# Performance work log

Hardware: AMD Instinct MI355X
Metric: run time of the kernel (lower is better)

## Reference

```python
import jax, jax.numpy as jnp
import numpy as np

B, S, D, O, H, E, K = 4, 1024, 1024, 1024, 2048, 8, 2
EPS = 1e-5

def _layernorm(x, g, b):
    m = jnp.mean(x, axis=-1, keepdims=True)
    v = jnp.mean(jnp.square(x - m), axis=-1, keepdims=True)
    return (x - m) * jax.lax.rsqrt(v + EPS) * g + b

def setup_inputs() -> dict:
    key = jax.random.key(0)
    ks = jax.random.split(key, 8)
    def xavier(k, shape):
        fan_out, fan_in = shape[-2], shape[-1]
        bound = float(np.sqrt(6.0 / (fan_in + fan_out)))
        return jax.random.uniform(k, shape, jnp.float32, -bound, bound)
    return {
        "x": jax.random.normal(ks[0], (B, S, D), jnp.float32),
        "ln1_g": jnp.ones((D,), jnp.float32), "ln1_b": jnp.zeros((D,), jnp.float32),
        "router_w": xavier(ks[1], (E, D)), "router_b": jnp.zeros((E,), jnp.float32),
        "sh_w1": xavier(ks[2], (H, D)), "sh_b1": jnp.zeros((H,), jnp.float32),
        "sh_w2": xavier(ks[3], (O, H)), "sh_b2": jnp.zeros((O,), jnp.float32),
        "e_w1": xavier(ks[4], (E, H, D)), "e_b1": jnp.zeros((E, H), jnp.float32),
        "e_w2": xavier(ks[5], (E, O, H)), "e_b2": jnp.zeros((E, O), jnp.float32),
        "ln2_g": jnp.ones((O,), jnp.float32), "ln2_b": jnp.zeros((O,), jnp.float32),
    }

def reference(x, ln1_g, ln1_b, router_w, router_b, sh_w1, sh_b1, sh_w2, sh_b2,
              e_w1, e_b1, e_w2, e_b2, ln2_g, ln2_b):
    # eval mode: no router noise, no aux loss
    x_norm = _layernorm(x, ln1_g, ln1_b)               # [B,S,D]
    xf = x_norm.reshape(-1, D)                          # [T,D]
    logits = xf @ router_w.T + router_b                 # [T,E]
    probs = jax.nn.softmax(logits, axis=-1)
    tk_w, tk_i = jax.lax.top_k(probs, K)                # [T,K]
    tk_w = tk_w / jnp.sum(tk_w, axis=-1, keepdims=True)
    # shared expert (exact GELU, as torch nn.GELU default)
    shared = jax.nn.gelu(xf @ sh_w1.T + sh_b1, approximate=False) @ sh_w2.T + sh_b2  # [T,O]
    # all experts densely, combined sparsely by top-k weights
    hid = jax.nn.gelu(jnp.einsum('td,ehd->teh', xf, e_w1) + e_b1, approximate=False)  # [T,E,H]
    eout = jnp.einsum('teh,eoh->teo', hid, e_w2) + e_b2                                # [T,E,O]
    comb_w = jnp.sum(jax.nn.one_hot(tk_i, E, dtype=xf.dtype) * tk_w[..., None], axis=1)  # [T,E]
    out = shared * (1.0 / (E + 1)) + jnp.einsum('te,teo->to', comb_w, eout)           # [T,O]
    out = _layernorm(out.reshape(B, S, O), ln2_g, ln2_b)
    return out
```

## Files before the change

kernel.cpp:

```cpp
#include <hip/hip_runtime.h>
#include <math.h>
#include <stdint.h>

typedef unsigned short u16;
typedef unsigned int u32;

typedef __attribute__((ext_vector_type(8))) short bf16x8;
typedef __attribute__((ext_vector_type(4))) float f32x4;

#define ASYNC_COPY16(g, l)                                                         \
  __builtin_amdgcn_global_load_lds((__attribute__((address_space(1))) const void*)(g), \
                                   (__attribute__((address_space(3))) void*)(l), 16, 0, 0)

__device__ __forceinline__ float bf2f(u16 u) {
  union { u32 i; float f; } v; v.i = ((u32)u) << 16; return v.f;
}
__device__ __forceinline__ u16 f2bf(float f) {
  union { float f; u32 i; } v; v.f = f;
  u32 r = v.i + 0x7fffu + ((v.i >> 16) & 1u);
  return (u16)(r >> 16);
}

__global__ __launch_bounds__(256) void cvt_all_k(
    const float* __restrict__ s0, const float* __restrict__ s1,
    const float* __restrict__ s2, const float* __restrict__ s3,
    u16* __restrict__ dst)
{
  const int64_t i0 = (int64_t)blockIdx.x * 2048 + (int64_t)threadIdx.x * 8;
  const float* src; int64_t rel;
  if (i0 < 2097152)       { src = s0; rel = i0; }
  else if (i0 < 4194304)  { src = s1; rel = i0 - 2097152; }
  else if (i0 < 20971520) { src = s2; rel = i0 - 4194304; }
  else                    { src = s3; rel = i0 - 20971520; }
  const float4 a = *(const float4*)(src + rel);
  const float4 b = *(const float4*)(src + rel + 4);
  union { u16 h[8]; uint4 v; } o;
  o.h[0] = f2bf(a.x); o.h[1] = f2bf(a.y); o.h[2] = f2bf(a.z); o.h[3] = f2bf(a.w);
  o.h[4] = f2bf(b.x); o.h[5] = f2bf(b.y); o.h[6] = f2bf(b.z); o.h[7] = f2bf(b.w);
  *(uint4*)(dst + i0) = o.v;
}

__global__ __launch_bounds__(256) void ln_router_k(
    const float* __restrict__ x, const float* __restrict__ g, const float* __restrict__ b,
    const float* __restrict__ rw, const float* __restrict__ rb,
    u16* __restrict__ xn, int* __restrict__ tk_idx, float* __restrict__ tk_w)
{
  const int t = blockIdx.x, tid = threadIdx.x;
  __shared__ float xs[1024];
  __shared__ float red[8];
  __shared__ float logits[8];
  const int wave = tid >> 6, lane = tid & 63;

  const float4 xv = *(const float4*)(x + (size_t)t * 1024 + 4 * tid);
  float v0 = xv.x, v1 = xv.y, v2 = xv.z, v3 = xv.w;
  float s = v0 + v1 + v2 + v3;
  float q = v0 * v0 + v1 * v1 + v2 * v2 + v3 * v3;
#pragma unroll
  for (int o = 32; o > 0; o >>= 1) { s += __shfl_down(s, o, 64); q += __shfl_down(q, o, 64); }
  if (lane == 0) { red[wave] = s; red[4 + wave] = q; }
  __syncthreads();
  if (tid == 0) {
    float S = red[0] + red[1] + red[2] + red[3];
    float Q = red[4] + red[5] + red[6] + red[7];
    float mean = S * (1.0f / 1024.0f);
    float var = Q * (1.0f / 1024.0f) - mean * mean;
    red[0] = mean; red[1] = rsqrtf(var + 1e-5f);
  }
  __syncthreads();
  const float mean = red[0], rstd = red[1];
  float vv[4] = {v0, v1, v2, v3};
  union { u16 h[4]; uint2 v; } pk;
#pragma unroll
  for (int j = 0; j < 4; ++j) {
    int d = 4 * tid + j;
    float y = (vv[j] - mean) * rstd * g[d] + b[d];
    xs[d] = y;
    pk.h[j] = f2bf(y);
  }
  *(uint2*)(xn + (size_t)t * 1024 + 4 * tid) = pk.v;
  __syncthreads();
#pragma unroll
  for (int pe = 0; pe < 2; ++pe) {
    int e = wave + 4 * pe;
    const float* wrow = rw + (size_t)e * 1024;
    float acc = 0.f;
#pragma unroll
    for (int j = 0; j < 16; ++j) {
      int d = lane + 64 * j;
      acc += xs[d] * wrow[d];
    }
#pragma unroll
    for (int o = 32; o > 0; o >>= 1) acc += __shfl_down(acc, o, 64);
    if (lane == 0) logits[e] = acc + rb[e];
  }
  __syncthreads();
  if (tid == 0) {
    int i0 = 0; float l0 = logits[0];
#pragma unroll
    for (int e = 1; e < 8; ++e) if (logits[e] > l0) { l0 = logits[e]; i0 = e; }
    int i1 = -1; float l1 = -3.4e38f;
#pragma unroll
    for (int e = 0; e < 8; ++e) { if (e == i0) continue; if (logits[e] > l1) { l1 = logits[e]; i1 = e; } }
    float w0 = 1.0f / (1.0f + expf(l1 - l0));
    float w1 = 1.0f - w0;
    tk_idx[2 * t] = i0; tk_idx[2 * t + 1] = i1;
    tk_w[2 * t] = w0; tk_w[2 * t + 1] = w1;
  }
}

__device__ __forceinline__ uint4 u4_add(uint4 a, uint4 b) {
  uint4 r; r.x = a.x + b.x; r.y = a.y + b.y; r.z = a.z + b.z; r.w = a.w + b.w; return r;
}
__device__ __forceinline__ uint4 u4_sub(uint4 a, uint4 b) {
  uint4 r; r.x = a.x - b.x; r.y = a.y - b.y; r.z = a.z - b.z; r.w = a.w - b.w; return r;
}

__global__ __launch_bounds__(256) void assign_k(
    const int* __restrict__ tk_idx, const float* __restrict__ tk_w,
    int* __restrict__ offs, int* __restrict__ slot_token,
    float* __restrict__ slot_w, int* __restrict__ slot_of)
{
  const int tid = threadIdx.x, lane = tid & 63, wave = tid >> 6;
  int eidx[32];
#pragma unroll
  for (int j = 0; j < 32; ++j) eidx[j] = tk_idx[tid * 32 + j];

  uint4 p = {0u, 0u, 0u, 0u};
#pragma unroll
  for (int j = 0; j < 32; ++j) {
    int e = eidx[j];
    unsigned inc = 1u << ((e & 1) * 16);
    int c = e >> 1;
    if (c == 0) p.x += inc; else if (c == 1) p.y += inc;
    else if (c == 2) p.z += inc; else p.w += inc;
  }
  const uint4 own = p;
#pragma unroll
  for (int o = 1; o < 64; o <<= 1) {
    uint4 t;
    t.x = (u32)__shfl_up((int)p.x, o, 64);
    t.y = (u32)__shfl_up((int)p.y, o, 64);
    t.z = (u32)__shfl_up((int)p.z, o, 64);
    t.w = (u32)__shfl_up((int)p.w, o, 64);
    if (lane >= o) p = u4_add(p, t);
  }
  __shared__ uint4 wtot[4];
  __shared__ int offs_s[9];
  if (lane == 63) wtot[wave] = p;
  __syncthreads();
  uint4 wbase = {0u, 0u, 0u, 0u};
  uint4 gtot = {0u, 0u, 0u, 0u};
#pragma unroll
  for (int w2 = 0; w2 < 4; ++w2) {
    uint4 t = wtot[w2];
    if (w2 < wave) wbase = u4_add(wbase, t);
    gtot = u4_add(gtot, t);
  }
  const uint4 excl = u4_sub(p, own);
  if (tid == 0) {
    int gtots[8] = { (int)(gtot.x & 0xffff), (int)(gtot.x >> 16),
                     (int)(gtot.y & 0xffff), (int)(gtot.y >> 16),
                     (int)(gtot.z & 0xffff), (int)(gtot.z >> 16),
                     (int)(gtot.w & 0xffff), (int)(gtot.w >> 16) };
    int a = 0;
#pragma unroll
    for (int e = 0; e < 8; ++e) { offs_s[e] = a; offs[e] = a; a += gtots[e]; }
    offs_s[8] = a; offs[8] = a;
  }
  __syncthreads();
  const uint4 pre = u4_add(wbase, excl);
  int base[8];
  base[0] = offs_s[0] + (int)(pre.x & 0xffff);
  base[1] = offs_s[1] + (int)(pre.x >> 16);
  base[2] = offs_s[2] + (int)(pre.y & 0xffff);
  base[3] = offs_s[3] + (int)(pre.y >> 16);
  base[4] = offs_s[4] + (int)(pre.z & 0xffff);
  base[5] = offs_s[5] + (int)(pre.z >> 16);
  base[6] = offs_s[6] + (int)(pre.w & 0xffff);
  base[7] = offs_s[7] + (int)(pre.w >> 16);
#pragma unroll
  for (int j = 0; j < 32; ++j) {
    int idx = tid * 32 + j;
    int e = eidx[j];
    int s = base[e]++;
    slot_token[s] = idx >> 1;
    slot_w[s] = tk_w[idx];
    slot_of[idx] = s;
  }
}

template <int N, int KD, int STAGE>
__global__ __launch_bounds__(256) void gemm_fused_k(
    const u16* __restrict__ Abase, const u16* __restrict__ Bsh,
    const u16* __restrict__ Bex, const float* __restrict__ bias_sh,
    const float* __restrict__ bias_ex,
    float* __restrict__ outF, u16* __restrict__ outH,
    const int* __restrict__ offs, const int* __restrict__ slot_token,
    const float* __restrict__ slot_w)
{
  const int tid = threadIdx.x;
  const int z = blockIdx.z;
  int off = 0, cnt = 4096, obase = 0;
  const u16* B = Bsh;
  const float* biasp = bias_sh;
  if (z > 0) {
    off = offs[z - 1]; cnt = offs[z] - off; obase = 4096 + off;
    B = Bex + (size_t)(z - 1) * N * KD;
    biasp = bias_ex + (size_t)(z - 1) * N;
  }
  const int m0 = blockIdx.y * 128;
  if (m0 >= cnt) return;
  const int n0 = blockIdx.x * 128;

  __shared__ u16 lA[128 * 32];
  __shared__ u16 lB[128 * 32];

  const int rS = tid >> 2;
  const int c8 = (tid & 3) * 8;

  int ra0 = m0 + rS;      if (ra0 > cnt - 1) ra0 = cnt - 1;
  int ra1 = m0 + rS + 64; if (ra1 > cnt - 1) ra1 = cnt - 1;
  size_t arow0, arow1;
  if (STAGE == 1) {
    if (z == 0) { arow0 = (size_t)ra0; arow1 = (size_t)ra1; }
    else        { arow0 = (size_t)slot_token[off + ra0]; arow1 = (size_t)slot_token[off + ra1]; }
  } else {
    if (z == 0) { arow0 = (size_t)ra0; arow1 = (size_t)ra1; }
    else        { arow0 = (size_t)(4096 + off + ra0); arow1 = (size_t)(4096 + off + ra1); }
  }
  const u16* gA0 = Abase + arow0 * KD + c8;
  const u16* gA1 = Abase + arow1 * KD + c8;
  const u16* gB0 = B + (size_t)(n0 + rS) * KD + c8;
  const u16* gB1 = B + (size_t)(n0 + rS + 64) * KD + c8;

  const int wave = tid >> 6, lane = tid & 63;
  u16* lA_w0 = lA + wave * 512;
  u16* lA_w1 = lA + 2048 + wave * 512;
  u16* lB_w0 = lB + wave * 512;
  u16* lB_w1 = lB + 2048 + wave * 512;

  const int wr = wave >> 1, wc = wave & 1;
  const int fr = lane & 15, fq = lane >> 4;
  const u16* rdA = lA + (wr * 64 + fr) * 32 + fq * 8;
  const u16* rdB = lB + (wc * 64 + fr) * 32 + fq * 8;

  f32x4 acc[4][4];
  const f32x4 zero = {0.f, 0.f, 0.f, 0.f};
#pragma unroll
  for (int i = 0; i < 4; ++i)
#pragma unroll
    for (int n = 0; n < 4; ++n) acc[i][n] = zero;

  const int NK = KD / 32;
  for (int kb = 0; kb < NK; ++kb) {
    __syncthreads();
    ASYNC_COPY16(gA0, lA_w0);
    ASYNC_COPY16(gA1, lA_w1);
    ASYNC_COPY16(gB0, lB_w0);
    ASYNC_COPY16(gB1, lB_w1);
    gA0 += 32; gA1 += 32; gB0 += 32; gB1 += 32;
    __syncthreads();
    bf16x8 af[4], bfv[4];
#pragma unroll
    for (int i = 0; i < 4; ++i) af[i] = *(const bf16x8*)(rdA + i * 16 * 32);
#pragma unroll
    for (int n = 0; n < 4; ++n) bfv[n] = *(const bf16x8*)(rdB + n * 16 * 32);
#pragma unroll
    for (int i = 0; i < 4; ++i)
#pragma unroll
      for (int n = 0; n < 4; ++n)
        acc[i][n] = __builtin_amdgcn_mfma_f32_16x16x32_bf16(af[i], bfv[n], acc[i][n], 0, 0, 0);
  }

  const int colBase = n0 + wc * 64;
#pragma unroll
  for (int i = 0; i < 4; ++i) {
    const int mlBase = m0 + wr * 64 + i * 16 + fq * 4;
#pragma unroll
    for (int r = 0; r < 4; ++r) {
      const int ml = mlBase + r;
      if (ml >= cnt) continue;
      const size_t orow = (size_t)(obase + ml) * N;
      float rwgt = (STAGE == 2) ? ((z == 0) ? (1.0f / 9.0f) : slot_w[off + ml]) : 1.f;
#pragma unroll
      for (int n = 0; n < 4; ++n) {
        const int col = colBase + n * 16 + fr;
        float v = acc[i][n][r] + biasp[col];
        if (STAGE == 1) {
          v = 0.5f * v * (1.0f + erff(v * 0.70710678118654752f));
          outH[orow + col] = f2bf(v);
        } else {
          outF[orow + col] = v * rwgt;
        }
      }
    }
  }
}

__global__ __launch_bounds__(256) void combine_ln2_k(
    const float* __restrict__ sh_out, const float* __restrict__ eout,
    const int* __restrict__ slot_of,
    const float* __restrict__ g2, const float* __restrict__ b2,
    float* __restrict__ out)
{
  const int t = blockIdx.x, tid = threadIdx.x;
  const int wave = tid >> 6, lane = tid & 63;
  __shared__ float red[8];
  const size_t s0 = (size_t)slot_of[2 * t], s1 = (size_t)slot_of[2 * t + 1];
  const float4 a  = *(const float4*)(sh_out + (size_t)t * 1024 + 4 * tid);
  const float4 c0 = *(const float4*)(eout + s0 * 1024 + 4 * tid);
  const float4 c1 = *(const float4*)(eout + s1 * 1024 + 4 * tid);
  float v0 = a.x + c0.x + c1.x;
  float v1 = a.y + c0.y + c1.y;
  float v2 = a.z + c0.z + c1.z;
  float v3 = a.w + c0.w + c1.w;
  float s = v0 + v1 + v2 + v3;
  float q = v0 * v0 + v1 * v1 + v2 * v2 + v3 * v3;
#pragma unroll
  for (int o = 32; o > 0; o >>= 1) { s += __shfl_down(s, o, 64); q += __shfl_down(q, o, 64); }
  if (lane == 0) { red[wave] = s; red[4 + wave] = q; }
  __syncthreads();
  if (tid == 0) {
    float S = red[0] + red[1] + red[2] + red[3];
    float Q = red[4] + red[5] + red[6] + red[7];
    float mean = S * (1.0f / 1024.0f);
    float var = Q * (1.0f / 1024.0f) - mean * mean;
    red[0] = mean; red[1] = rsqrtf(var + 1e-5f);
  }
  __syncthreads();
  const float mean = red[0], rstd = red[1];
  float vv[4] = {v0, v1, v2, v3};
#pragma unroll
  for (int j = 0; j < 4; ++j) {
    int d = 4 * tid + j;
    out[(size_t)t * 1024 + d] = (vv[j] - mean) * rstd * g2[d] + b2[d];
  }
}

extern "C" void kernel_launch(void* const* d_in, const int* in_sizes, int n_in,
                              void* d_out, int out_size, void* d_ws, size_t ws_size,
                              hipStream_t stream)
{
  const float* x     = (const float*)d_in[0];
  const float* ln1_g = (const float*)d_in[1];
  const float* ln1_b = (const float*)d_in[2];
  const float* rw    = (const float*)d_in[3];
  const float* rb    = (const float*)d_in[4];
  const float* sh_w1 = (const float*)d_in[5];
  const float* sh_b1 = (const float*)d_in[6];
  const float* sh_w2 = (const float*)d_in[7];
  const float* sh_b2 = (const float*)d_in[8];
  const float* e_w1  = (const float*)d_in[9];
  const float* e_b1  = (const float*)d_in[10];
  const float* e_w2  = (const float*)d_in[11];
  const float* e_b2  = (const float*)d_in[12];
  const float* ln2_g = (const float*)d_in[13];
  const float* ln2_b = (const float*)d_in[14];
  float* out = (float*)d_out;

  char* w = (char*)d_ws;
  u16*   x_norm = (u16*)(w + 0);
  u16*   hid    = (u16*)(w + (8u << 20));
  float* outb   = (float*)(w + (56u << 20));
  u16*   w1b    = (u16*)(w + (104u << 20));
  u16*   w2b    = (u16*)(w + (108u << 20));
  u16*   ew1b   = (u16*)(w + (112u << 20));
  u16*   ew2b   = (u16*)(w + (144u << 20));
  char*  meta   = w + (176u << 20);
  int*   tk_idx     = (int*)(meta);
  float* tk_w       = (float*)(meta + (32u << 10));
  int*   slot_token = (int*)(meta + (64u << 10));
  float* slot_w     = (float*)(meta + (96u << 10));
  int*   slot_of    = (int*)(meta + (128u << 10));
  int*   offs       = (int*)(meta + (160u << 10));

  cvt_all_k<<<18432, 256, 0, stream>>>(sh_w1, sh_w2, e_w1, e_w2, w1b);

  ln_router_k<<<4096, 256, 0, stream>>>(x, ln1_g, ln1_b, rw, rb, x_norm, tk_idx, tk_w);
  assign_k<<<1, 256, 0, stream>>>(tk_idx, tk_w, offs, slot_token, slot_w, slot_of);

  gemm_fused_k<2048, 1024, 1><<<dim3(16, 32, 9), 256, 0, stream>>>(
      x_norm, w1b, ew1b, sh_b1, e_b1, nullptr, hid, offs, slot_token, nullptr);
  gemm_fused_k<1024, 2048, 2><<<dim3(8, 32, 9), 256, 0, stream>>>(
      hid, w2b, ew2b, sh_b2, e_b2, outb, nullptr, offs, slot_token, slot_w);

  combine_ln2_k<<<4096, 256, 0, stream>>>(outb, outb + (size_t)4096 * 1024,
                                          slot_of, ln2_g, ln2_b, out);
}
```

Baseline: 445.8 us.

## Double-buffer GEMM LDS tiles, use tanh-form GELU, store stage-2 outputs as bf16

The GEMM main loop now uses two LDS buffers and prefetches the next K-slice while computing the current one, leaving one barrier per iteration instead of two. The exact erf GELU becomes a sigmoid-based tanh approximation built on __expf. Stage-2 partial outputs are written as bf16 instead of fp32, halving the writes and the combine kernel's reads. The trade-off is more numerical error from the approximate GELU and the bf16 intermediates, plus a possible race: the single barrier may not wait for the async LDS copies to complete before they are read.

```diff
diff --git a/kernel.cpp b/kernel.cpp
--- a/kernel.cpp
+++ b/kernel.cpp
@@ -19,6 +19,11 @@
   union { float f; u32 i; } v; v.f = f;
   u32 r = v.i + 0x7fffu + ((v.i >> 16) & 1u);
   return (u16)(r >> 16);
+}
+__device__ __forceinline__ float gelu_fast(float x) {
+  float t = x * x;
+  float z = 1.5957691f * x * (1.0f + 0.044715f * t);
+  return x / (1.0f + __expf(-z));
 }
 
 __global__ __launch_bounds__(256) void cvt_all_k(
@@ -194,7 +199,7 @@
     const u16* __restrict__ Abase, const u16* __restrict__ Bsh,
     const u16* __restrict__ Bex, const float* __restrict__ bias_sh,
     const float* __restrict__ bias_ex,
-    float* __restrict__ outF, u16* __restrict__ outH,
+    u16* __restrict__ outH,
     const int* __restrict__ offs, const int* __restrict__ slot_token,
     const float* __restrict__ slot_w)
 {
@@ -212,8 +217,8 @@
   if (m0 >= cnt) return;
   const int n0 = blockIdx.x * 128;
 
-  __shared__ u16 lA[128 * 32];
-  __shared__ u16 lB[128 * 32];
+  __shared__ u16 lA[2][4096];
+  __shared__ u16 lB[2][4096];
 
   const int rS = tid >> 2;
   const int c8 = (tid & 3) * 8;
@@ -234,15 +239,8 @@
   const u16* gB1 = B + (size_t)(n0 + rS + 64) * KD + c8;
 
   const int wave = tid >> 6, lane = tid & 63;
-  u16* lA_w0 = lA + wave * 512;
-  u16* lA_w1 = lA + 2048 + wave * 512;
-  u16* lB_w0 = lB + wave * 512;
-  u16* lB_w1 = lB + 2048 + wave * 512;
-
   const int wr = wave >> 1, wc = wave & 1;
   const int fr = lane & 15, fq = lane >> 4;
-  const u16* rdA = lA + (wr * 64 + fr) * 32 + fq * 8;
-  const u16* rdB = lB + (wc * 64 + fr) * 32 + fq * 8;
 
   f32x4 acc[4][4];
   const f32x4 zero = {0.f, 0.f, 0.f, 0.f};
@@ -252,14 +250,26 @@
     for (int n = 0; n < 4; ++n) acc[i][n] = zero;
 
   const int NK = KD / 32;
+  {
+    ASYNC_COPY16(gA0, &lA[0][0] + wave * 512);
+    ASYNC_COPY16(gA1, &lA[0][0] + 2048 + wave * 512);
+    ASYNC_COPY16(gB0, &lB[0][0] + wave * 512);
+    ASYNC_COPY16(gB1, &lB[0][0] + 2048 + wave * 512);
+    gA0 += 32; gA1 += 32; gB0 += 32; gB1 += 32;
+  }
+
   for (int kb = 0; kb < NK; ++kb) {
+    const int cur = kb & 1;
     __syncthreads();
-    ASYNC_COPY16(gA0, lA_w0);
-    ASYNC_COPY16(gA1, lA_w1);
-    ASYNC_COPY16(gB0, lB_w0);
-    ASYNC_COPY16(gB1, lB_w1);
-    gA0 += 32; gA1 += 32; gB0 += 32; gB1 += 32;
-    __syncthreads();
+    if (kb + 1 < NK) {
+      ASYNC_COPY16(gA0, &lA[cur ^ 1][0] + wave * 512);
+      ASYNC_COPY16(gA1, &lA[cur ^ 1][0] + 2048 + wave * 512);
+      ASYNC_COPY16(gB0, &lB[cur ^ 1][0] + wave * 512);
+      ASYNC_COPY16(gB1, &lB[cur ^ 1][0] + 2048 + wave * 512);
+      gA0 += 32; gA1 += 32; gB0 += 32; gB1 += 32;
+    }
+    const u16* rdA = &lA[cur][0] + (wr * 64 + fr) * 32 + fq * 8;
+    const u16* rdB = &lB[cur][0] + (wc * 64 + fr) * 32 + fq * 8;
     bf16x8 af[4], bfv[4];
 #pragma unroll
     for (int i = 0; i < 4; ++i) af[i] = *(const bf16x8*)(rdA + i * 16 * 32);
@@ -286,19 +296,16 @@
       for (int n = 0; n < 4; ++n) {
         const int col = colBase + n * 16 + fr;
         float v = acc[i][n][r] + biasp[col];
-        if (STAGE == 1) {
-          v = 0.5f * v * (1.0f + erff(v * 0.70710678118654752f));
-          outH[orow + col] = f2bf(v);
-        } else {
-          outF[orow + col] = v * rwgt;
-        }
+        if (STAGE == 1) v = gelu_fast(v);
+        else            v = v * rwgt;
+        outH[orow + col] = f2bf(v);
       }
     }
   }
 }
 
 __global__ __launch_bounds__(256) void combine_ln2_k(
-    const float* __restrict__ sh_out, const float* __restrict__ eout,
+    const u16* __restrict__ sh_out, const u16* __restrict__ eout,
     const int* __restrict__ slot_of,
     const float* __restrict__ g2, const float* __restrict__ b2,
     float* __restrict__ out)
@@ -307,15 +314,15 @@
   const int wave = tid >> 6, lane = tid & 63;
   __shared__ float red[8];
   const size_t s0 = (size_t)slot_of[2 * t], s1 = (size_t)slot_of[2 * t + 1];
-  const float4 a  = *(const float4*)(sh_out + (size_t)t * 1024 + 4 * tid);
-  const float4 c0 = *(const float4*)(eout + s0 * 1024 + 4 * tid);
-  const float4 c1 = *(const float4*)(eout + s1 * 1024 + 4 * tid);
-  float v0 = a.x + c0.x + c1.x;
-  float v1 = a.y + c0.y + c1.y;
-  float v2 = a.z + c0.z + c1.z;
-  float v3 = a.w + c0.w + c1.w;
-  float s = v0 + v1 + v2 + v3;
-  float q = v0 * v0 + v1 * v1 + v2 * v2 + v3 * v3;
+  union { uint2 v; u16 h[4]; } a, c0, c1;
+  a.v  = *(const uint2*)(sh_out + (size_t)t * 1024 + 4 * tid);
+  c0.v = *(const uint2*)(eout + s0 * 1024 + 4 * tid);
+  c1.v = *(const uint2*)(eout + s1 * 1024 + 4 * tid);
+  float vv[4];
+#pragma unroll
+  for (int j = 0; j < 4; ++j) vv[j] = bf2f(a.h[j]) + bf2f(c0.h[j]) + bf2f(c1.h[j]);
+  float s = vv[0] + vv[1] + vv[2] + vv[3];
+  float q = vv[0] * vv[0] + vv[1] * vv[1] + vv[2] * vv[2] + vv[3] * vv[3];
 #pragma unroll
   for (int o = 32; o > 0; o >>= 1) { s += __shfl_down(s, o, 64); q += __shfl_down(q, o, 64); }
   if (lane == 0) { red[wave] = s; red[4 + wave] = q; }
@@ -329,7 +336,6 @@
   }
   __syncthreads();
   const float mean = red[0], rstd = red[1];
-  float vv[4] = {v0, v1, v2, v3};
 #pragma unroll
   for (int j = 0; j < 4; ++j) {
     int d = 4 * tid + j;
@@ -361,7 +367,7 @@
   char* w = (char*)d_ws;
   u16*   x_norm = (u16*)(w + 0);
   u16*   hid    = (u16*)(w + (8u << 20));
-  float* outb   = (float*)(w + (56u << 20));
+  u16*   outb   = (u16*)(w + (56u << 20));
   u16*   w1b    = (u16*)(w + (104u << 20));
   u16*   w2b    = (u16*)(w + (108u << 20));
   u16*   ew1b   = (u16*)(w + (112u << 20));
@@ -380,9 +386,9 @@
   assign_k<<<1, 256, 0, stream>>>(tk_idx, tk_w, offs, slot_token, slot_w, slot_of);
 
   gemm_fused_k<2048, 1024, 1><<<dim3(16, 32, 9), 256, 0, stream>>>(
-      x_norm, w1b, ew1b, sh_b1, e_b1, nullptr, hid, offs, slot_token, nullptr);
+      x_norm, w1b, ew1b, sh_b1, e_b1, hid, offs, slot_token, nullptr);
   gemm_fused_k<1024, 2048, 2><<<dim3(8, 32, 9), 256, 0, stream>>>(
-      hid, w2b, ew2b, sh_b2, e_b2, outb, nullptr, offs, slot_token, slot_w);
+      hid, w2b, ew2b, sh_b2, e_b2, outb, offs, slot_token, slot_w);
 
   combine_ln2_k<<<4096, 256, 0, stream>>>(outb, outb + (size_t)4096 * 1024,
                                           slot_of, ln2_g, ln2_b, out);
```

Result: no change. 438.6 us (-1.6%).
